# Kernel optimization log

Measured on AMD Instinct MI355X. Metric: run time of the kernel, lower is better.

## Reference

```python
import jax, jax.numpy as jnp
import numpy as np

N_USER, N_ITEM, D, K, E = 80000, 40000, 128, 10, 2000000

def _mlp(x, w1, b1, w2, b2, w3, b3):
    # MLP from source: linear->tanh->linear->tanh->linear->L2 normalize (eval mode, dropout off)
    x = jnp.tanh(x @ w1 + b1)
    x = jnp.tanh(x @ w2 + b2)
    x = x @ w3 + b3
    return x / jnp.maximum(jnp.linalg.norm(x, axis=-1, keepdims=True), 1e-12)

def setup_inputs() -> dict:
    key = jax.random.key(0)
    ks = jax.random.split(key, 24)
    s = 0.05
    inp = {
        'uemb_s': jax.random.normal(ks[0], (N_USER, D), jnp.float32),
        'iemb_s': jax.random.normal(ks[1], (N_ITEM, D), jnp.float32),
        'uemb_t': jax.random.normal(ks[2], (N_USER, D), jnp.float32),
        'u_emb_sp': jax.random.normal(ks[3], (N_USER, D), jnp.float32),
        'edge_user': jax.random.randint(ks[4], (E,), 0, N_USER, jnp.int32),
        'edge_item': jax.random.randint(ks[5], (E,), 0, N_ITEM, jnp.int32),
        # meta nets
        'Wu': jax.random.normal(ks[6], (4 * D, D), jnp.float32) * s,
        'bu': jnp.zeros((D,), jnp.float32),
        'Wi': jax.random.normal(ks[7], (2 * D, D), jnp.float32) * s,
        'bi': jnp.zeros((D,), jnp.float32),
        # mlp1: D -> D*K -> D//2 -> D*K
        'm1w1': jax.random.normal(ks[8], (D, D * K), jnp.float32) * s,
        'm1b1': jnp.zeros((D * K,), jnp.float32),
        'm1w2': jax.random.normal(ks[9], (D * K, D // 2), jnp.float32) * s,
        'm1b2': jnp.zeros((D // 2,), jnp.float32),
        'm1w3': jax.random.normal(ks[10], (D // 2, D * K), jnp.float32) * s,
        'm1b3': jnp.zeros((D * K,), jnp.float32),
        # mlp2: D -> D*K -> D//2 -> D*K
        'm2w1': jax.random.normal(ks[11], (D, D * K), jnp.float32) * s,
        'm2b1': jnp.zeros((D * K,), jnp.float32),
        'm2w2': jax.random.normal(ks[12], (D * K, D // 2), jnp.float32) * s,
        'm2b2': jnp.zeros((D // 2,), jnp.float32),
        'm2w3': jax.random.normal(ks[13], (D // 2, D * K), jnp.float32) * s,
        'm2b3': jnp.zeros((D * K,), jnp.float32),
    }
    return inp

def reference(uemb_s, iemb_s, uemb_t, u_emb_sp, edge_user, edge_item,
              Wu, bu, Wi, bi,
              m1w1, m1b1, m1w2, m1b2, m1w3, m1b3,
              m2w1, m2b1, m2w2, m2b2, m2w3, m2b3):
    # spmm with all-ones values == gather + segment_sum over the bipartite edge list
    neighbors_u = jax.ops.segment_sum(iemb_s[edge_item], edge_user, num_segments=N_USER)  # [U, D]
    tmp_embu = jax.lax.stop_gradient(
        jnp.concatenate([uemb_s, uemb_t, u_emb_sp, neighbors_u], axis=1)) @ Wu + bu       # [U, D]
    neighbors_i = jax.ops.segment_sum(((uemb_s + u_emb_sp) * 0.5)[edge_user], edge_item,
                                      num_segments=N_ITEM)                               # [I, D]
    tmp_embi = jax.lax.stop_gradient(
        jnp.concatenate([iemb_s, neighbors_i], axis=1)) @ Wi + bi                         # [I, D]
    metau = _mlp(tmp_embu, m1w1, m1b1, m1w2, m1b2, m1w3, m1b3).reshape(-1, D, K)          # [U, D, K]
    metai = _mlp(tmp_embi, m2w1, m2b1, m2w2, m2b2, m2w3, m2b3).reshape(-1, K, D)          # [I, K, D]
    meta_biasu = jnp.mean(metau, axis=0)  # [D, K]
    meta_biasi = jnp.mean(metai, axis=0)  # [K, D]
    low_weightu = jax.nn.softmax(metau + meta_biasu, axis=1)
    low_weighti = jax.nn.softmax(metai + meta_biasi, axis=1)
    return (low_weightu, low_weighti)
```

## Files before the change

kernel.cpp:

```cpp
#include <hip/hip_runtime.h>
#include <hip/hip_bf16.h>

#define D_ 128
#define DK_ 1280
#define K_ 10

typedef __attribute__((ext_vector_type(8))) short bh8;
typedef __attribute__((ext_vector_type(4))) short bh4;
typedef __attribute__((ext_vector_type(4))) float f32x4;

__device__ __forceinline__ short f2b(float f) {
    unsigned u = __builtin_bit_cast(unsigned, f);
    u += 0x7fffu + ((u >> 16) & 1u);
    return (short)(u >> 16);
}
__device__ __forceinline__ float b2f(short s) {
    unsigned u = ((unsigned)(unsigned short)s) << 16;
    return __builtin_bit_cast(float, u);
}
__device__ __forceinline__ float tanh_fast(float x) {
    float e = __expf(2.f * x);
    return 1.f - __fdividef(2.f, e + 1.f);
}
__device__ __forceinline__ f32x4 mfma16(bh8 a, bh8 b, f32x4 c) {
    return __builtin_amdgcn_mfma_f32_16x16x32_bf16(a, b, c, 0, 0, 0);
}

__device__ __forceinline__ int blk_excl_scan(int v, int t) {
    __shared__ int wp[4];
    int lane = t & 63, w = t >> 6;
    int s = v;
    for (int o = 1; o < 64; o <<= 1) {
        int pv = __shfl_up(s, o);
        if (lane >= o) s += pv;
    }
    if (lane == 63) wp[w] = s;
    __syncthreads();
    if (t == 0) {
        int a = 0;
#pragma unroll
        for (int k = 0; k < 4; ++k) { int x = wp[k]; wp[k] = a; a += x; }
    }
    __syncthreads();
    int r = s - v + wp[w];
    __syncthreads();
    return r;
}

__global__ __launch_bounds__(256) void cvt_all(
    const float* __restrict__ us, const float* __restrict__ ut,
    const float* __restrict__ usp, const float* __restrict__ is_,
    short* __restrict__ usb, short* __restrict__ utb,
    short* __restrict__ uspb, short* __restrict__ uavg, short* __restrict__ isb,
    int n4u, int n4i)
{
    int i = blockIdx.x * 256 + threadIdx.x;
    if (i < n4u) {
        float4 a = ((const float4*)us)[i];
        float4 b = ((const float4*)ut)[i];
        float4 c = ((const float4*)usp)[i];
        bh4 sa, sb, sc, sv;
        sa[0] = f2b(a.x); sa[1] = f2b(a.y); sa[2] = f2b(a.z); sa[3] = f2b(a.w);
        sb[0] = f2b(b.x); sb[1] = f2b(b.y); sb[2] = f2b(b.z); sb[3] = f2b(b.w);
        sc[0] = f2b(c.x); sc[1] = f2b(c.y); sc[2] = f2b(c.z); sc[3] = f2b(c.w);
        sv[0] = f2b(0.5f * (a.x + c.x)); sv[1] = f2b(0.5f * (a.y + c.y));
        sv[2] = f2b(0.5f * (a.z + c.z)); sv[3] = f2b(0.5f * (a.w + c.w));
        ((bh4*)usb)[i] = sa; ((bh4*)utb)[i] = sb;
        ((bh4*)uspb)[i] = sc; ((bh4*)uavg)[i] = sv;
    } else if (i < n4u + n4i) {
        int j = i - n4u;
        float4 v = ((const float4*)is_)[j];
        bh4 s;
        s[0] = f2b(v.x); s[1] = f2b(v.y); s[2] = f2b(v.z); s[3] = f2b(v.w);
        ((bh4*)isb)[j] = s;
    }
}

struct PackArgs {
    const float* W[8];
    short* o[8];
    int K[8];
    int N[8];
};
__global__ __launch_bounds__(256) void pack_all(PackArgs pa)
{
    int seg = blockIdx.y;
    int K = pa.K[seg], N = pa.N[seg];
    int total = K * N;
    int o = blockIdx.x * 256 + threadIdx.x;
    if (o >= total) return;
    const float* W = pa.W[seg];
    short* out = pa.o[seg];
    int j    = o & 7;
    int lane = (o >> 3) & 63;
    int rest = o >> 9;
    int KK = K >> 5;
    int kk = rest % KK;
    int tile = rest / KK;
    int k = kk * 32 + (lane >> 4) * 8 + j;
    int n = tile * 16 + (lane & 15);
    out[o] = f2b(W[(size_t)k * N + n]);
}

__global__ __launch_bounds__(256) void bhist_kernel(
    const int* __restrict__ eu, const int* __restrict__ ei,
    int* __restrict__ bcu, int* __restrict__ bci,
    int E, int shu, int shi, int nbu, int nbi)
{
    __shared__ int hu[160], hi[160];
    int t = threadIdx.x;
    int base = blockIdx.x * 4096;
    if (t < 160) { hu[t] = 0; hi[t] = 0; }
    __syncthreads();
    int n = min(4096, E - base);
#pragma unroll 4
    for (int k = 0; k < 16; ++k) {
        int idx = k * 256 + t;
        if (idx < n) {
            atomicAdd(&hu[eu[base + idx] >> shu], 1);
            atomicAdd(&hi[ei[base + idx] >> shi], 1);
        }
    }
    __syncthreads();
    if (t < nbu && hu[t]) atomicAdd(&bcu[t], hu[t]);
    if (t < nbi && hi[t]) atomicAdd(&bci[t], hi[t]);
}

__global__ __launch_bounds__(256) void binit_kernel(
    const int* __restrict__ bcu, int* __restrict__ gcu, int* __restrict__ bbu, int nbu,
    const int* __restrict__ bci, int* __restrict__ gci, int* __restrict__ bbi, int nbi,
    int E)
{
    int t = threadIdx.x;
    {
        int v = (t < nbu) ? bcu[t] : 0;
        int ex = blk_excl_scan(v, t);
        if (t < nbu) { gcu[t] = ex; bbu[t] = ex; }
        if (t == 0) bbu[nbu] = E;
    }
    __syncthreads();
    {
        int v = (t < nbi) ? bci[t] : 0;
        int ex = blk_excl_scan(v, t);
        if (t < nbi) { gci[t] = ex; bbi[t] = ex; }
        if (t == 0) bbi[nbi] = E;
    }
}

__global__ __launch_bounds__(256) void partition_kernel(
    const int* __restrict__ eu, const int* __restrict__ ei,
    int* __restrict__ gcu, int* __restrict__ gci,
    uint2* __restrict__ ebu, uint2* __restrict__ ebi,
    int E, int shu, int shi, int nbu, int nbi)
{
    __shared__ int hu[160], hi[160];
    int t = threadIdx.x;
    int base = blockIdx.x * 4096;
    if (t < 160) { hu[t] = 0; hi[t] = 0; }
    __syncthreads();
    int n = min(4096, E - base);
    int us[16], is_[16];
#pragma unroll 4
    for (int k = 0; k < 16; ++k) {
        int idx = k * 256 + t;
        if (idx < n) {
            us[k] = eu[base + idx];
            is_[k] = ei[base + idx];
            atomicAdd(&hu[us[k] >> shu], 1);
            atomicAdd(&hi[is_[k] >> shi], 1);
        } else us[k] = -1;
    }
    __syncthreads();
    if (t < nbu) { int c = hu[t]; hu[t] = c ? atomicAdd(&gcu[t], c) : 0; }
    if (t < nbi) { int c = hi[t]; hi[t] = c ? atomicAdd(&gci[t], c) : 0; }
    __syncthreads();
#pragma unroll 4
    for (int k = 0; k < 16; ++k) {
        if (us[k] >= 0) {
            int p1 = atomicAdd(&hu[us[k] >> shu], 1);
            ebu[p1] = make_uint2((unsigned)us[k], (unsigned)is_[k]);
            int p2 = atomicAdd(&hi[is_[k] >> shi], 1);
            ebi[p2] = make_uint2((unsigned)is_[k], (unsigned)us[k]);
        }
    }
}

__global__ __launch_bounds__(256) void fill2_all(
    const uint2* __restrict__ ebu, const int* __restrict__ bbu,
    int* __restrict__ off_u, int* __restrict__ end_u, int* __restrict__ adj_u,
    int NBU, int U,
    const uint2* __restrict__ ebi, const int* __restrict__ bbi,
    int* __restrict__ off_i, int* __restrict__ end_i, int* __restrict__ adj_i, int I)
{
    __shared__ int lcnt[512];
    __shared__ int lcur[512];
    bool isU = (int)blockIdx.x < NBU;
    const uint2* ebuf = isU ? ebu : ebi;
    const int* bbase  = isU ? bbu : bbi;
    int* off  = isU ? off_u : off_i;
    int* end_ = isU ? end_u : end_i;
    int* adj  = isU ? adj_u : adj_i;
    int span_sh = isU ? 9 : 8;
    int nrows = isU ? U : I;
    int b = isU ? blockIdx.x : blockIdx.x - NBU;

    int t = threadIdx.x;
    int rbase = b << span_sh;
    int span = min(1 << span_sh, nrows - rbase);
    int regbeg = bbase[b], regend = bbase[b + 1];
    for (int j = t; j < span; j += 256) lcnt[j] = 0;
    __syncthreads();
    for (int e = regbeg + t; e < regend; e += 256)
        atomicAdd(&lcnt[ebuf[e].x - rbase], 1);
    __syncthreads();
    int c0 = (2 * t < span) ? lcnt[2 * t] : 0;
    int c1 = (2 * t + 1 < span) ? lcnt[2 * t + 1] : 0;
    int ex = blk_excl_scan(c0 + c1, t);
    if (2 * t < span) {
        int beg = regbeg + ex;
        off[rbase + 2 * t] = beg;
        end_[rbase + 2 * t] = beg + c0;
        lcur[2 * t] = beg;
    }
    if (2 * t + 1 < span) {
        int beg = regbeg + ex + c0;
        off[rbase + 2 * t + 1] = beg;
        end_[rbase + 2 * t + 1] = beg + c1;
        lcur[2 * t + 1] = beg;
    }
    __syncthreads();
    for (int e = regbeg + t; e < regend; e += 256) {
        uint2 p = ebuf[e];
        int slot = atomicAdd(&lcur[p.x - rbase], 1);
        adj[slot] = (int)p.y;
    }
}

__global__ __launch_bounds__(256) void gather_all(
    const short* __restrict__ embU, const short* __restrict__ embI,
    const int* __restrict__ off_u, const int* __restrict__ end_u, const int* __restrict__ adj_u,
    const int* __restrict__ off_i, const int* __restrict__ end_i, const int* __restrict__ adj_i,
    short* __restrict__ nub, short* __restrict__ nib, int U, int I)
{
    int gw = (blockIdx.x * 256 + threadIdx.x) >> 6;
    int lane = threadIdx.x & 63;
    const short* emb; const int *offp, *endp, *adjp; short* outp; int row;
    if (gw < U)          { emb = embU; offp = off_u; endp = end_u; adjp = adj_u; outp = nub; row = gw; }
    else if (gw < U + I) { emb = embI; offp = off_i; endp = end_i; adjp = adj_i; outp = nib; row = gw - U; }
    else return;

    int beg = offp[row], end = endp[row];
    float ax = 0.f, ay = 0.f;
    int j = beg;
    for (; j + 3 < end; j += 4) {
        unsigned a = *(const unsigned*)(emb + (size_t)adjp[j]     * D_ + lane * 2);
        unsigned b = *(const unsigned*)(emb + (size_t)adjp[j + 1] * D_ + lane * 2);
        unsigned c = *(const unsigned*)(emb + (size_t)adjp[j + 2] * D_ + lane * 2);
        unsigned d = *(const unsigned*)(emb + (size_t)adjp[j + 3] * D_ + lane * 2);
        ax += b2f((short)(a & 0xffff)) + b2f((short)(b & 0xffff))
            + b2f((short)(c & 0xffff)) + b2f((short)(d & 0xffff));
        ay += b2f((short)(a >> 16)) + b2f((short)(b >> 16))
            + b2f((short)(c >> 16)) + b2f((short)(d >> 16));
    }
    for (; j < end; ++j) {
        unsigned a = *(const unsigned*)(emb + (size_t)adjp[j] * D_ + lane * 2);
        ax += b2f((short)(a & 0xffff));
        ay += b2f((short)(a >> 16));
    }
    unsigned o = ((unsigned)(unsigned short)f2b(ay) << 16) | (unsigned short)(unsigned)f2b(ax);
    *(unsigned*)(outp + (size_t)row * D_ + lane * 2) = o;
}

struct MlpArgs {
    const short *uA0, *uA1, *uA2, *uA3;
    const short *iA0, *iA1;
    const short *uWg, *uW1, *uW2, *uW3;
    const short *iWg, *iW1, *iW2, *iW3;
    const float *ubg, *ub1, *ub2, *ub3;
    const float *ibg, *ib1, *ib2, *ib3;
    short *uY, *iY;
    int UB;
};

#define X2ST 136
#define H1ST 1288
#define H2ST 72

__global__ __launch_bounds__(256, 3) void fused_mlp_all(MlpArgs P)
{
    __shared__ char pool[48128];
    short* x2   = (short*)pool;
    short* h2   = (short*)(pool + 4352);
    float* wred = (float*)(pool + 6656);
    short* xc   = (short*)(pool + 6912);
    short* h1   = (short*)(pool + 6912);

    const int t = threadIdx.x;
    const int l = t & 63;
    const int w = t >> 6;
    const int lr = l & 15;
    const int lg = l >> 4;

    const bool isU = (int)blockIdx.x < P.UB;
    const int bid = isU ? (int)blockIdx.x : (int)blockIdx.x - P.UB;
    const size_t rb0 = (size_t)bid * 16;
    const int CHSH = isU ? 6 : 5;
    const int KKG  = isU ? 16 : 8;
    const int XST  = isU ? 520 : 264;
    const short* Wg = isU ? P.uWg : P.iWg;
    const short* W1 = isU ? P.uW1 : P.iW1;
    const short* W2 = isU ? P.uW2 : P.iW2;
    const short* W3 = isU ? P.uW3 : P.iW3;
    const float* bg = isU ? P.ubg : P.ibg;
    const float* b1 = isU ? P.ub1 : P.ib1;
    const float* b2 = isU ? P.ub2 : P.ib2;
    const float* b3 = isU ? P.ub3 : P.ib3;
    short* Ybf = isU ? P.uY : P.iY;

    for (int idx = t; idx < (16 << CHSH); idx += 256) {
        int row = idx >> CHSH;
        int slot = idx & ((1 << CHSH) - 1);
        int a = slot >> 4, cs = slot & 15;
        const short* src = isU ? (a == 0 ? P.uA0 : a == 1 ? P.uA1 : a == 2 ? P.uA2 : P.uA3)
                               : (a == 0 ? P.iA0 : P.iA1);
        bh8 v = *(const bh8*)(src + (rb0 + row) * D_ + cs * 8);
        *(bh8*)(xc + row * XST + slot * 8) = v;
    }
    __syncthreads();

    {
        f32x4 accA0 = {0,0,0,0}, accB0 = accA0, accA1 = accA0, accB1 = accA0;
#pragma unroll 4
        for (int kk = 0; kk < KKG; ++kk) {
            bh8 xf = *(const bh8*)(xc + lr * XST + kk * 32 + lg * 8);
            bh8 w0 = *(const bh8*)(Wg + (((size_t)(2 * w)     * KKG + kk) * 64 + l) * 8);
            bh8 w1 = *(const bh8*)(Wg + (((size_t)(2 * w + 1) * KKG + kk) * 64 + l) * 8);
            if (kk & 1) { accB0 = mfma16(w0, xf, accB0); accB1 = mfma16(w1, xf, accB1); }
            else        { accA0 = mfma16(w0, xf, accA0); accA1 = mfma16(w1, xf, accA1); }
        }
        const float* bp0 = bg + (2 * w) * 16 + lg * 4;
        const float* bp1 = bg + (2 * w + 1) * 16 + lg * 4;
        bh4 p0, p1;
#pragma unroll
        for (int r = 0; r < 4; ++r) {
            p0[r] = f2b(accA0[r] + accB0[r] + bp0[r]);
            p1[r] = f2b(accA1[r] + accB1[r] + bp1[r]);
        }
        *(bh4*)(x2 + lr * X2ST + (2 * w) * 16 + lg * 4) = p0;
        *(bh4*)(x2 + lr * X2ST + (2 * w + 1) * 16 + lg * 4) = p1;
    }
    __syncthreads();

    {
        bh8 xf[4];
#pragma unroll
        for (int kk = 0; kk < 4; ++kk)
            xf[kk] = *(const bh8*)(x2 + lr * X2ST + kk * 32 + lg * 8);
#pragma unroll 2
        for (int tile = w * 20; tile < w * 20 + 20; ++tile) {
            f32x4 acc = {0, 0, 0, 0};
#pragma unroll
            for (int kk = 0; kk < 4; ++kk) {
                bh8 wf = *(const bh8*)(W1 + (((size_t)tile * 4 + kk) * 64 + l) * 8);
                acc = mfma16(wf, xf[kk], acc);
            }
            const float* bp = b1 + tile * 16 + lg * 4;
            bh4 pk;
#pragma unroll
            for (int r = 0; r < 4; ++r) pk[r] = f2b(tanh_fast(acc[r] + bp[r]));
            *(bh4*)(h1 + lr * H1ST + tile * 16 + lg * 4) = pk;
        }
    }
    __syncthreads();

    {
        f32x4 accA = {0,0,0,0}, accB = accA;
#pragma unroll 4
        for (int kk = 0; kk < 40; ++kk) {
            bh8 hf = *(const bh8*)(h1 + lr * H1ST + kk * 32 + lg * 8);
            bh8 wf = *(const bh8*)(W2 + (((size_t)w * 40 + kk) * 64 + l) * 8);
            if (kk & 1) accB = mfma16(wf, hf, accB);
            else        accA = mfma16(wf, hf, accA);
        }
        const float* bp = b2 + w * 16 + lg * 4;
        bh4 pk;
#pragma unroll
        for (int r = 0; r < 4; ++r) pk[r] = f2b(tanh_fast(accA[r] + accB[r] + bp[r]));
        *(bh4*)(h2 + lr * H2ST + w * 16 + lg * 4) = pk;
    }
    __syncthreads();

    {
        bh8 hf0 = *(const bh8*)(h2 + lr * H2ST + lg * 8);
        bh8 hf1 = *(const bh8*)(h2 + lr * H2ST + 32 + lg * 8);
        float ssq = 0.f;
#pragma unroll 2
        for (int tile = w * 20; tile < w * 20 + 20; ++tile) {
            f32x4 acc = {0, 0, 0, 0};
            bh8 w0 = *(const bh8*)(W3 + (((size_t)tile * 2 + 0) * 64 + l) * 8);
            bh8 w1 = *(const bh8*)(W3 + (((size_t)tile * 2 + 1) * 64 + l) * 8);
            acc = mfma16(w0, hf0, acc);
            acc = mfma16(w1, hf1, acc);
            const float* bp = b3 + tile * 16 + lg * 4;
            bh4 pk;
#pragma unroll
            for (int r = 0; r < 4; ++r) {
                float v = acc[r] + bp[r];
                ssq = fmaf(v, v, ssq);
                pk[r] = f2b(v);
            }
            *(bh4*)(h1 + lr * H1ST + tile * 16 + lg * 4) = pk;
        }
        ssq += __shfl_xor(ssq, 16);
        ssq += __shfl_xor(ssq, 32);
        if (l < 16) wred[w * 16 + l] = ssq;
    }
    __syncthreads();

    {
        float s = wred[lr] + wred[16 + lr] + wred[32 + lr] + wred[48 + lr];
        float nrm = 1.f / fmaxf(sqrtf(s), 1e-12f);
        short* dst = Ybf + (rb0 + lr) * DK_;
#pragma unroll 2
        for (int tile = w * 20; tile < w * 20 + 20; ++tile) {
            bh4 pk = *(const bh4*)(h1 + lr * H1ST + tile * 16 + lg * 4);
            bh4 o;
#pragma unroll
            for (int r = 0; r < 4; ++r) o[r] = f2b(b2f(pk[r]) * nrm);
            *(bh4*)(dst + tile * 16 + lg * 4) = o;
        }
    }
}

__global__ __launch_bounds__(256) void finalize_bias(
    const short* __restrict__ Yu, const short* __restrict__ Yi,
    float* __restrict__ bsu, float* __restrict__ bsi, int U, int I, int NCH)
{
    int z = blockIdx.y;
    const short* Y = z ? Yi : Yu;
    float* dst = z ? bsi : bsu;
    int M = z ? I : U;
    int chunk = (M + NCH - 1) / NCH;
    int r0 = blockIdx.x * chunk;
    int r1 = min(M, r0 + chunk);
    if (r0 >= r1) return;
    int t = threadIdx.x;
    float s0 = 0.f, s1 = 0.f, s2 = 0.f, s3 = 0.f, s4 = 0.f;
    for (int r = r0; r < r1; ++r) {
        const short* row = Y + (size_t)r * DK_;
        s0 += b2f(row[t]);
        s1 += b2f(row[256 + t]);
        s2 += b2f(row[512 + t]);
        s3 += b2f(row[768 + t]);
        s4 += b2f(row[1024 + t]);
    }
    atomicAdd(&dst[t], s0);
    atomicAdd(&dst[256 + t], s1);
    atomicAdd(&dst[512 + t], s2);
    atomicAdd(&dst[768 + t], s3);
    atomicAdd(&dst[1024 + t], s4);
}

__global__ __launch_bounds__(64) void softmax_all(
    const short* __restrict__ Yu, const short* __restrict__ Yi,
    const float* __restrict__ bsu, const float* __restrict__ bsi,
    float invU, float invI,
    float* __restrict__ outu, float* __restrict__ outi, int U, int I)
{
    __shared__ float rowb[DK_];
    int b = blockIdx.x;
    int t = threadIdx.x;
    if (b < U) {
        size_t base = (size_t)b * DK_;
        for (int i = t; i < DK_ / 4; i += 64) {
            uint2 a = ((const uint2*)(Yu + base))[i];
            float4 bv = ((const float4*)bsu)[i];
            rowb[4 * i + 0] = b2f((short)(a.x & 0xffff)) + bv.x * invU;
            rowb[4 * i + 1] = b2f((short)(a.x >> 16))    + bv.y * invU;
            rowb[4 * i + 2] = b2f((short)(a.y & 0xffff)) + bv.z * invU;
            rowb[4 * i + 3] = b2f((short)(a.y >> 16))    + bv.w * invU;
        }
        __syncthreads();
#pragma unroll 1
        for (int k = 0; k < K_; ++k) {
            float v0 = rowb[t * K_ + k];
            float v1 = rowb[(t + 64) * K_ + k];
            float m = fmaxf(v0, v1);
            for (int off = 32; off; off >>= 1) m = fmaxf(m, __shfl_xor(m, off));
            float e0 = expf(v0 - m), e1 = expf(v1 - m);
            float s = e0 + e1;
            for (int off = 32; off; off >>= 1) s += __shfl_xor(s, off);
            float rs = 1.f / s;
            rowb[t * K_ + k] = e0 * rs;
            rowb[(t + 64) * K_ + k] = e1 * rs;
        }
        __syncthreads();
        for (int i = t; i < DK_ / 4; i += 64)
            ((float4*)(outu + base))[i] = ((const float4*)rowb)[i];
    } else {
        int it = b - U;
        if (it >= I) return;
        size_t base = (size_t)it * DK_;
        float v0[K_], v1[K_];
        float m0 = -1e30f, m1 = -1e30f;
#pragma unroll
        for (int k = 0; k < K_; ++k) {
            unsigned a = *(const unsigned*)(Yi + base + k * D_ + 2 * t);
            float2 bv = ((const float2*)(bsi + k * D_))[t];
            v0[k] = b2f((short)(a & 0xffff)) + bv.x * invI;
            v1[k] = b2f((short)(a >> 16))    + bv.y * invI;
            m0 = fmaxf(m0, v0[k]); m1 = fmaxf(m1, v1[k]);
        }
        float s0 = 0.f, s1 = 0.f;
#pragma unroll
        for (int k = 0; k < K_; ++k) {
            v0[k] = expf(v0[k] - m0); s0 += v0[k];
            v1[k] = expf(v1[k] - m1); s1 += v1[k];
        }
        float r0 = 1.f / s0, r1 = 1.f / s1;
#pragma unroll
        for (int k = 0; k < K_; ++k) {
            float2 o; o.x = v0[k] * r0; o.y = v1[k] * r1;
            ((float2*)(outi + base + k * D_))[t] = o;
        }
    }
}

extern "C" void kernel_launch(void* const* d_in, const int* in_sizes, int n_in,
                              void* d_out, int out_size, void* d_ws, size_t ws_size,
                              hipStream_t stream)
{
    const float* uemb_s   = (const float*)d_in[0];
    const float* iemb_s   = (const float*)d_in[1];
    const float* uemb_t   = (const float*)d_in[2];
    const float* u_emb_sp = (const float*)d_in[3];
    const int*   eu       = (const int*)d_in[4];
    const int*   ei       = (const int*)d_in[5];
    const float* Wu  = (const float*)d_in[6];
    const float* bu  = (const float*)d_in[7];
    const float* Wi  = (const float*)d_in[8];
    const float* bi  = (const float*)d_in[9];
    const float* m1w1 = (const float*)d_in[10];
    const float* m1b1 = (const float*)d_in[11];
    const float* m1w2 = (const float*)d_in[12];
    const float* m1b2 = (const float*)d_in[13];
    const float* m1w3 = (const float*)d_in[14];
    const float* m1b3 = (const float*)d_in[15];
    const float* m2w1 = (const float*)d_in[16];
    const float* m2b1 = (const float*)d_in[17];
    const float* m2w2 = (const float*)d_in[18];
    const float* m2b2 = (const float*)d_in[19];
    const float* m2w3 = (const float*)d_in[20];
    const float* m2b3 = (const float*)d_in[21];

    const int U = in_sizes[0] / D_;
    const int I = in_sizes[1] / D_;
    const int E = in_sizes[4];

    const int SHU = 9, SHI = 8;
    const int NBU = (U + 511) >> 9;
    const int NBI = (I + 255) >> 8;
    const int UB = U / 16, IB = I / 16;

    char* p = (char*)d_ws;
    auto alloc = [&](size_t bytes) { char* r = p; p += (bytes + 255) & ~(size_t)255; return r; };

    short* usb  = (short*)alloc((size_t)U * D_ * 2);
    short* utb  = (short*)alloc((size_t)U * D_ * 2);
    short* uspb = (short*)alloc((size_t)U * D_ * 2);
    short* uavg = (short*)alloc((size_t)U * D_ * 2);
    short* isb  = (short*)alloc((size_t)I * D_ * 2);
    short* nub  = (short*)alloc((size_t)U * D_ * 2);
    short* nib  = (short*)alloc((size_t)I * D_ * 2);
    short* ybu  = (short*)alloc((size_t)U * DK_ * 2);
    short* ybi  = (short*)alloc((size_t)I * DK_ * 2);
    short* WgU  = (short*)alloc(512 * 128 * 2);
    short* WgI  = (short*)alloc(256 * 128 * 2);
    short* W1U  = (short*)alloc(128 * 1280 * 2);
    short* W2U  = (short*)alloc(1280 * 64 * 2);
    short* W3U  = (short*)alloc(64 * 1280 * 2);
    short* W1I  = (short*)alloc(128 * 1280 * 2);
    short* W2I  = (short*)alloc(1280 * 64 * 2);
    short* W3I  = (short*)alloc(64 * 1280 * 2);
    int*   zbuf = (int*)alloc((320 + 2 * DK_) * 4);
    int* bcnt_u = zbuf;
    int* bcnt_i = zbuf + 160;
    float* bsu  = (float*)(zbuf + 320);
    float* bsi  = bsu + DK_;
    int* gcur_u = (int*)alloc(160 * 4);
    int* gcur_i = (int*)alloc(160 * 4);
    int* bbase_u = (int*)alloc(161 * 4);
    int* bbase_i = (int*)alloc(161 * 4);
    int* off_u  = (int*)alloc((size_t)U * 4);
    int* end_u  = (int*)alloc((size_t)U * 4);
    int* off_i  = (int*)alloc((size_t)I * 4);
    int* end_i  = (int*)alloc((size_t)I * 4);
    uint2* ebu  = (uint2*)alloc((size_t)E * 8);
    uint2* ebi  = (uint2*)alloc((size_t)E * 8);
    int* adj_u  = (int*)alloc((size_t)E * 4);
    int* adj_i  = (int*)alloc((size_t)E * 4);

    float* outu = (float*)d_out;
    float* outi = outu + (size_t)U * DK_;

    hipMemsetAsync(zbuf, 0, (320 + 2 * DK_) * 4, stream);

    int n4u = U * D_ / 4, n4i = I * D_ / 4;
    cvt_all<<<(n4u + n4i + 255) / 256, 256, 0, stream>>>(
        uemb_s, uemb_t, u_emb_sp, iemb_s, usb, utb, uspb, uavg, isb, n4u, n4i);

    PackArgs pa;
    pa.W[0] = Wu;   pa.o[0] = WgU; pa.K[0] = 512;  pa.N[0] = 128;
    pa.W[1] = Wi;   pa.o[1] = WgI; pa.K[1] = 256;  pa.N[1] = 128;
    pa.W[2] = m1w1; pa.o[2] = W1U; pa.K[2] = 128;  pa.N[2] = 1280;
    pa.W[3] = m1w2; pa.o[3] = W2U; pa.K[3] = 1280; pa.N[3] = 64;
    pa.W[4] = m1w3; pa.o[4] = W3U; pa.K[4] = 64;   pa.N[4] = 1280;
    pa.W[5] = m2w1; pa.o[5] = W1I; pa.K[5] = 128;  pa.N[5] = 1280;
    pa.W[6] = m2w2; pa.o[6] = W2I; pa.K[6] = 1280; pa.N[6] = 64;
    pa.W[7] = m2w3; pa.o[7] = W3I; pa.K[7] = 64;   pa.N[7] = 1280;
    pack_all<<<dim3(640, 8), 256, 0, stream>>>(pa);

    int pb = (E + 4095) / 4096;
    bhist_kernel<<<pb, 256, 0, stream>>>(eu, ei, bcnt_u, bcnt_i, E, SHU, SHI, NBU, NBI);
    binit_kernel<<<1, 256, 0, stream>>>(bcnt_u, gcur_u, bbase_u, NBU,
                                        bcnt_i, gcur_i, bbase_i, NBI, E);
    partition_kernel<<<pb, 256, 0, stream>>>(eu, ei, gcur_u, gcur_i, ebu, ebi,
                                             E, SHU, SHI, NBU, NBI);
    fill2_all<<<NBU + NBI, 256, 0, stream>>>(ebu, bbase_u, off_u, end_u, adj_u, NBU, U,
                                             ebi, bbase_i, off_i, end_i, adj_i, I);

    gather_all<<<(U + I + 3) / 4, 256, 0, stream>>>(
        isb, uavg, off_u, end_u, adj_u, off_i, end_i, adj_i, nub, nib, U, I);

    MlpArgs ma;
    ma.uA0 = usb; ma.uA1 = utb; ma.uA2 = uspb; ma.uA3 = nub;
    ma.iA0 = isb; ma.iA1 = nib;
    ma.uWg = WgU; ma.uW1 = W1U; ma.uW2 = W2U; ma.uW3 = W3U;
    ma.iWg = WgI; ma.iW1 = W1I; ma.iW2 = W2I; ma.iW3 = W3I;
    ma.ubg = bu; ma.ub1 = m1b1; ma.ub2 = m1b2; ma.ub3 = m1b3;
    ma.ibg = bi; ma.ib1 = m2b1; ma.ib2 = m2b2; ma.ib3 = m2b3;
    ma.uY = ybu; ma.iY = ybi;
    ma.UB = UB;
    fused_mlp_all<<<UB + IB, 256, 0, stream>>>(ma);

    finalize_bias<<<dim3(256, 2), 256, 0, stream>>>(ybu, ybi, bsu, bsi, U, I, 256);

    softmax_all<<<U + I, 64, 0, stream>>>(ybu, ybi, bsu, bsi,
                                          1.0f / (float)U, 1.0f / (float)I, outu, outi, U, I);
}
```

Baseline: 1.027 ms.

## Split MLP hidden layer into halves to shrink LDS and raise occupancy

```diff
diff --git a/kernel.cpp b/kernel.cpp
--- a/kernel.cpp
+++ b/kernel.cpp
@@ -282,18 +282,15 @@
     int UB;
 };
 
-#define X2ST 136
-#define H1ST 1288
-#define H2ST 72
-
-__global__ __launch_bounds__(256, 3) void fused_mlp_all(MlpArgs P)
-{
-    __shared__ char pool[48128];
+__global__ __launch_bounds__(256, 4) void fused_mlp_all(MlpArgs P)
+{
+    __shared__ char pool[27712];
     short* x2   = (short*)pool;
     short* h2   = (short*)(pool + 4352);
     float* wred = (float*)(pool + 6656);
-    short* xc   = (short*)(pool + 6912);
-    short* h1   = (short*)(pool + 6912);
+    float* nrms = (float*)(pool + 6912);
+    short* xc   = (short*)(pool + 6976);
+    short* h1h  = (short*)(pool + 6976);
 
     const int t = threadIdx.x;
     const int l = t & 63;
@@ -329,105 +326,124 @@
     __syncthreads();
 
     {
-        f32x4 accA0 = {0,0,0,0}, accB0 = accA0, accA1 = accA0, accB1 = accA0;
-#pragma unroll 4
+        f32x4 a0 = {0,0,0,0}, b0 = a0, a1 = a0, b1v = a0;
+        const short* wp = Wg + (size_t)(2 * w) * KKG * 512 + l * 8;
+        const short* wq = wp + (size_t)KKG * 512;
+        const short* xp = xc + lr * XST + lg * 8;
         for (int kk = 0; kk < KKG; ++kk) {
-            bh8 xf = *(const bh8*)(xc + lr * XST + kk * 32 + lg * 8);
-            bh8 w0 = *(const bh8*)(Wg + (((size_t)(2 * w)     * KKG + kk) * 64 + l) * 8);
-            bh8 w1 = *(const bh8*)(Wg + (((size_t)(2 * w + 1) * KKG + kk) * 64 + l) * 8);
-            if (kk & 1) { accB0 = mfma16(w0, xf, accB0); accB1 = mfma16(w1, xf, accB1); }
-            else        { accA0 = mfma16(w0, xf, accA0); accA1 = mfma16(w1, xf, accA1); }
-        }
-        const float* bp0 = bg + (2 * w) * 16 + lg * 4;
-        const float* bp1 = bg + (2 * w + 1) * 16 + lg * 4;
+            bh8 xf = *(const bh8*)xp; xp += 32;
+            bh8 w0 = *(const bh8*)wp; wp += 512;
+            bh8 w1 = *(const bh8*)wq; wq += 512;
+            if (kk & 1) { b0 = mfma16(w0, xf, b0); b1v = mfma16(w1, xf, b1v); }
+            else        { a0 = mfma16(w0, xf, a0); a1 = mfma16(w1, xf, a1); }
+        }
+        float4 c0 = *(const float4*)(bg + (2 * w) * 16 + lg * 4);
+        float4 c1 = *(const float4*)(bg + (2 * w + 1) * 16 + lg * 4);
         bh4 p0, p1;
-#pragma unroll
-        for (int r = 0; r < 4; ++r) {
-            p0[r] = f2b(accA0[r] + accB0[r] + bp0[r]);
-            p1[r] = f2b(accA1[r] + accB1[r] + bp1[r]);
-        }
-        *(bh4*)(x2 + lr * X2ST + (2 * w) * 16 + lg * 4) = p0;
-        *(bh4*)(x2 + lr * X2ST + (2 * w + 1) * 16 + lg * 4) = p1;
-    }
-    __syncthreads();
-
-    {
-        bh8 xf[4];
-#pragma unroll
-        for (int kk = 0; kk < 4; ++kk)
-            xf[kk] = *(const bh8*)(x2 + lr * X2ST + kk * 32 + lg * 8);
+        p0[0] = f2b(a0[0] + b0[0] + c0.x); p0[1] = f2b(a0[1] + b0[1] + c0.y);
+        p0[2] = f2b(a0[2] + b0[2] + c0.z); p0[3] = f2b(a0[3] + b0[3] + c0.w);
+        p1[0] = f2b(a1[0] + b1v[0] + c1.x); p1[1] = f2b(a1[1] + b1v[1] + c1.y);
+        p1[2] = f2b(a1[2] + b1v[2] + c1.z); p1[3] = f2b(a1[3] + b1v[3] + c1.w);
+        *(bh4*)(x2 + lr * 136 + (2 * w) * 16 + lg * 4) = p0;
+        *(bh4*)(x2 + lr * 136 + (2 * w + 1) * 16 + lg * 4) = p1;
+    }
+    __syncthreads();
+
+    bh8 xf[4];
+#pragma unroll
+    for (int kk = 0; kk < 4; ++kk)
+        xf[kk] = *(const bh8*)(x2 + lr * 136 + kk * 32 + lg * 8);
+
+    f32x4 c2a = {0,0,0,0}, c2b = c2a;
+#pragma unroll 1
+    for (int h = 0; h < 2; ++h) {
+        const short* wp = W1 + (size_t)(h * 40 + w * 10) * 2048 + l * 8;
+        const float* bp = b1 + (h * 40 + w * 10) * 16 + lg * 4;
+        short* hp = h1h + lr * 648 + w * 160 + lg * 4;
 #pragma unroll 2
-        for (int tile = w * 20; tile < w * 20 + 20; ++tile) {
+        for (int tt = 0; tt < 10; ++tt) {
             f32x4 acc = {0, 0, 0, 0};
 #pragma unroll
             for (int kk = 0; kk < 4; ++kk) {
-                bh8 wf = *(const bh8*)(W1 + (((size_t)tile * 4 + kk) * 64 + l) * 8);
+                bh8 wf = *(const bh8*)wp; wp += 512;
                 acc = mfma16(wf, xf[kk], acc);
             }
-            const float* bp = b1 + tile * 16 + lg * 4;
-            bh4 pk;
-#pragma unroll
-            for (int r = 0; r < 4; ++r) pk[r] = f2b(tanh_fast(acc[r] + bp[r]));
-            *(bh4*)(h1 + lr * H1ST + tile * 16 + lg * 4) = pk;
-        }
-    }
-    __syncthreads();
+            float4 bv = *(const float4*)bp; bp += 16;
+            bh4 pk1;
+            pk1[0] = f2b(tanh_fast(acc[0] + bv.x));
+            pk1[1] = f2b(tanh_fast(acc[1] + bv.y));
+            pk1[2] = f2b(tanh_fast(acc[2] + bv.z));
+            pk1[3] = f2b(tanh_fast(acc[3] + bv.w));
+            *(bh4*)hp = pk1; hp += 16;
+        }
+        __syncthreads();
+        const short* wp2 = W2 + (size_t)(w * 40 + h * 20) * 512 + l * 8;
+        const short* hq = h1h + lr * 648 + lg * 8;
+#pragma unroll 4
+        for (int kk = 0; kk < 20; ++kk) {
+            bh8 hf = *(const bh8*)hq; hq += 32;
+            bh8 wf = *(const bh8*)wp2; wp2 += 512;
+            if (kk & 1) c2b = mfma16(wf, hf, c2b);
+            else        c2a = mfma16(wf, hf, c2a);
+        }
+        __syncthreads();
+    }
 
     {
-        f32x4 accA = {0,0,0,0}, accB = accA;
-#pragma unroll 4
-        for (int kk = 0; kk < 40; ++kk) {
-            bh8 hf = *(const bh8*)(h1 + lr * H1ST + kk * 32 + lg * 8);
-            bh8 wf = *(const bh8*)(W2 + (((size_t)w * 40 + kk) * 64 + l) * 8);
-            if (kk & 1) accB = mfma16(wf, hf, accB);
-            else        accA = mfma16(wf, hf, accA);
-        }
-        const float* bp = b2 + w * 16 + lg * 4;
-        bh4 pk;
-#pragma unroll
-        for (int r = 0; r < 4; ++r) pk[r] = f2b(tanh_fast(accA[r] + accB[r] + bp[r]));
-        *(bh4*)(h2 + lr * H2ST + w * 16 + lg * 4) = pk;
-    }
-    __syncthreads();
-
+        float4 bv = *(const float4*)(b2 + w * 16 + lg * 4);
+        bh4 p2;
+        p2[0] = f2b(tanh_fast(c2a[0] + c2b[0] + bv.x));
+        p2[1] = f2b(tanh_fast(c2a[1] + c2b[1] + bv.y));
+        p2[2] = f2b(tanh_fast(c2a[2] + c2b[2] + bv.z));
+        p2[3] = f2b(tanh_fast(c2a[3] + c2b[3] + bv.w));
+        *(bh4*)(h2 + lr * 72 + w * 16 + lg * 4) = p2;
+    }
+    __syncthreads();
+
+    bh8 hf0 = *(const bh8*)(h2 + lr * 72 + lg * 8);
+    bh8 hf1 = *(const bh8*)(h2 + lr * 72 + 32 + lg * 8);
+    bh4 pk[20];
+    float ssq = 0.f;
     {
-        bh8 hf0 = *(const bh8*)(h2 + lr * H2ST + lg * 8);
-        bh8 hf1 = *(const bh8*)(h2 + lr * H2ST + 32 + lg * 8);
-        float ssq = 0.f;
-#pragma unroll 2
-        for (int tile = w * 20; tile < w * 20 + 20; ++tile) {
+        const short* wp3 = W3 + (size_t)(w * 20) * 1024 + l * 8;
+        const float* bp3 = b3 + w * 320 + lg * 4;
+#pragma unroll
+        for (int tt = 0; tt < 20; ++tt) {
             f32x4 acc = {0, 0, 0, 0};
-            bh8 w0 = *(const bh8*)(W3 + (((size_t)tile * 2 + 0) * 64 + l) * 8);
-            bh8 w1 = *(const bh8*)(W3 + (((size_t)tile * 2 + 1) * 64 + l) * 8);
+            bh8 w0 = *(const bh8*)(wp3 + tt * 1024);
+            bh8 w1 = *(const bh8*)(wp3 + tt * 1024 + 512);
             acc = mfma16(w0, hf0, acc);
             acc = mfma16(w1, hf1, acc);
-            const float* bp = b3 + tile * 16 + lg * 4;
-            bh4 pk;
-#pragma unroll
-            for (int r = 0; r < 4; ++r) {
-                float v = acc[r] + bp[r];
-                ssq = fmaf(v, v, ssq);
-                pk[r] = f2b(v);
-            }
-            *(bh4*)(h1 + lr * H1ST + tile * 16 + lg * 4) = pk;
-        }
-        ssq += __shfl_xor(ssq, 16);
-        ssq += __shfl_xor(ssq, 32);
-        if (l < 16) wred[w * 16 + l] = ssq;
+            float4 bv = *(const float4*)(bp3 + tt * 16);
+            float v0 = acc[0] + bv.x, v1 = acc[1] + bv.y;
+            float v2 = acc[2] + bv.z, v3 = acc[3] + bv.w;
+            ssq = fmaf(v0, v0, ssq); ssq = fmaf(v1, v1, ssq);
+            ssq = fmaf(v2, v2, ssq); ssq = fmaf(v3, v3, ssq);
+            bh4 o;
+            o[0] = f2b(v0); o[1] = f2b(v1); o[2] = f2b(v2); o[3] = f2b(v3);
+            pk[tt] = o;
+        }
+    }
+    ssq += __shfl_xor(ssq, 16);
+    ssq += __shfl_xor(ssq, 32);
+    if (l < 16) wred[w * 16 + l] = ssq;
+    __syncthreads();
+    if (t < 16) {
+        float s = wred[t] + wred[16 + t] + wred[32 + t] + wred[48 + t];
+        nrms[t] = 1.f / fmaxf(sqrtf(s), 1e-12f);
     }
     __syncthreads();
 
     {
-        float s = wred[lr] + wred[16 + lr] + wred[32 + lr] + wred[48 + lr];
-        float nrm = 1.f / fmaxf(sqrtf(s), 1e-12f);
-        short* dst = Ybf + (rb0 + lr) * DK_;
-#pragma unroll 2
-        for (int tile = w * 20; tile < w * 20 + 20; ++tile) {
-            bh4 pk = *(const bh4*)(h1 + lr * H1ST + tile * 16 + lg * 4);
+        float nrm = nrms[lr];
+        short* dst = Ybf + (rb0 + lr) * DK_ + w * 320 + lg * 4;
+#pragma unroll
+        for (int tt = 0; tt < 20; ++tt) {
+            bh4 pkv = pk[tt];
             bh4 o;
-#pragma unroll
-            for (int r = 0; r < 4; ++r) o[r] = f2b(b2f(pk[r]) * nrm);
-            *(bh4*)(dst + tile * 16 + lg * 4) = o;
+            o[0] = f2b(b2f(pkv[0]) * nrm); o[1] = f2b(b2f(pkv[1]) * nrm);
+            o[2] = f2b(b2f(pkv[2]) * nrm); o[3] = f2b(b2f(pkv[3]) * nrm);
+            *(bh4*)(dst + tt * 16) = o;
         }
     }
 }
```

Result: no change. 1.033 ms (+0.5%).
